# Performance work log

Measured on AMD Instinct MI355X. Metric: run time of the kernel, lower is better.

## Reference

```python
import jax, jax.numpy as jnp
import numpy as np

EPS = 1e-6
TEMPERATURE = 0.75
SINKHORN_ITERS = 7


def setup_inputs() -> dict:
    key = jax.random.key(0)
    ks = jax.random.split(key, 6)
    b, h, t, d_h = 4, 8, 4096, 64
    bs = 256
    nb = t // bs
    q = jax.random.normal(ks[0], (b, h, t, d_h), jnp.float32)
    k = jax.random.normal(ks[1], (b, h, t, d_h), jnp.float32)
    v = jax.random.normal(ks[2], (b, h, t, d_h), jnp.float32)
    # uniform noise for gumbel sampling in the sinkhorn sort net
    gumbel_u = jax.random.uniform(ks[3], (b * h, nb, nb), jnp.float32,
                                  minval=EPS, maxval=1.0 - EPS)
    W_out = jax.random.normal(ks[4], (2 * d_h, d_h), jnp.float32) / np.sqrt(2 * d_h)
    b_out = jnp.zeros((d_h,), jnp.float32)
    return {"q": q, "k": k, "v": v, "gumbel_u": gumbel_u,
            "W_out": W_out, "b_out": b_out, "bucket_size": bs}


def _sinkhorn(r, n_iters):
    # iterative row/col log-normalization of log-scores r: [bh, nb, nb]
    def body(r, _):
        r = r - jax.scipy.special.logsumexp(r, axis=2, keepdims=True)
        r = r - jax.scipy.special.logsumexp(r, axis=1, keepdims=True)
        return r, None
    r, _ = jax.lax.scan(body, r, None, length=n_iters)
    return jnp.exp(r)


def reference(q, k, v, gumbel_u, W_out, b_out, bucket_size):
    b, h, t, d_h = q.shape
    bh = b * h
    nb = t // bucket_size
    scale = d_h ** -0.5
    # merge batch/head and bucket: [bh, nb, bs, d_h]
    bq = q.reshape(bh, nb, bucket_size, d_h)
    bk = k.reshape(bh, nb, bucket_size, d_h)
    bv = v.reshape(bh, nb, bucket_size, d_h)
    # AttentionSortNet: bucket sums -> scores -> gumbel sinkhorn soft permutation
    q_sum = bq.sum(axis=2)  # [bh, nb, d_h]
    k_sum = bk.sum(axis=2)
    R0 = jax.nn.relu(jnp.einsum('bie,bje->bij', q_sum, k_sum) * scale)
    gumbel = -jnp.log(-jnp.log(gumbel_u + EPS) + EPS)
    r = (jnp.log(R0 + EPS) + gumbel) / TEMPERATURE
    R = _sinkhorn(r, SINKHORN_ITERS)  # [bh, nb, nb]
    # soft-reorder k/v buckets with R
    k_r = jnp.einsum('bij,bjsd->bisd', R, bk)
    v_r = jnp.einsum('bij,bjsd->bisd', R, bv)
    # local (within-bucket) attention
    local_s = jnp.einsum('bnie,bnje->bnij', bq, bk) * scale
    local_out = jnp.einsum('bnij,bnjd->bnid', jax.nn.softmax(local_s, axis=-1), bv)
    # attention over soft-sorted buckets
    sort_s = jnp.einsum('bnie,bnje->bnij', bq, k_r) * scale
    sort_out = jnp.einsum('bnij,bnjd->bnid', jax.nn.softmax(sort_s, axis=-1), v_r)
    # concat local + sorted heads, project 2*d_h -> d_h
    out = jnp.concatenate([local_out, sort_out], axis=-1)  # [bh, nb, bs, 2*d_h]
    out = out @ W_out + b_out
    return out.reshape(b, h, t, d_h)
```

## Files before the change

kernel.cpp:

```cpp
#include <hip/hip_runtime.h>
#include <math.h>


typedef __attribute__((ext_vector_type(8))) short short8;
typedef __attribute__((ext_vector_type(4))) float f32x4;

constexpr int BH = 32;
constexpr int NB = 16;
constexpr int BS = 256;
constexpr int D  = 64;
constexpr int BUCKET = BS * D;
constexpr float SCALE = 0.125f;

__device__ inline unsigned bf16_rne_u(float x) {
  unsigned u = __builtin_bit_cast(unsigned, x);
  return (u + 0x7FFFu + ((u >> 16) & 1u)) >> 16;
}
__device__ inline unsigned cvt2_bf16(float a, float b) {
  return bf16_rne_u(a) | (bf16_rne_u(b) << 16);
}
__device__ inline void split_pair(float a, float b, unsigned& uhi, unsigned& ulo) {
  uhi = cvt2_bf16(a, b);
  float ha = __builtin_bit_cast(float, uhi << 16);
  float hb = __builtin_bit_cast(float, uhi & 0xFFFF0000u);
  ulo = cvt2_bf16(a - ha, b - hb);
}

__global__ __launch_bounds__(256) void k_bucket_sums(
    const float* __restrict__ q, const float* __restrict__ k,
    float* __restrict__ qsum, float* __restrict__ ksum) {
  const int bid = blockIdx.x;
  const int t = threadIdx.x;
  const int c4 = t & 15;
  const int rg = t >> 4;
  const float4* qb = (const float4*)(q + (size_t)bid * BUCKET);
  const float4* kb = (const float4*)(k + (size_t)bid * BUCKET);
  float4 sq = make_float4(0.f, 0.f, 0.f, 0.f);
  float4 sk = make_float4(0.f, 0.f, 0.f, 0.f);
  for (int s = rg; s < BS; s += 16) {
    float4 a = qb[s * 16 + c4];
    float4 b2 = kb[s * 16 + c4];
    sq.x += a.x; sq.y += a.y; sq.z += a.z; sq.w += a.w;
    sk.x += b2.x; sk.y += b2.y; sk.z += b2.z; sk.w += b2.w;
  }
  __shared__ float red[2][16][64];
  *(float4*)&red[0][rg][4 * c4] = sq;
  *(float4*)&red[1][rg][4 * c4] = sk;
  __syncthreads();
  if (t < 128) {
    const int which = t >> 6;
    const int d = t & 63;
    float s = 0.f;
    #pragma unroll
    for (int g2 = 0; g2 < 16; ++g2) s += red[which][g2][d];
    (which ? ksum : qsum)[bid * D + d] = s;
  }
}

__global__ __launch_bounds__(256) void k_sinkhorn(
    const float* __restrict__ qsum, const float* __restrict__ ksum,
    const float* __restrict__ gu, float* __restrict__ R) {
  const int bh = blockIdx.x;
  const int t = threadIdx.x;
  const int i = t >> 4, j = t & 15;
  __shared__ float qs[16][64], ks[16][64], r[16][17];
  for (int idx = t; idx < NB * D; idx += 256) {
    qs[idx >> 6][idx & 63] = qsum[bh * NB * D + idx];
    ks[idx >> 6][idx & 63] = ksum[bh * NB * D + idx];
  }
  __syncthreads();
  float dot = 0.f;
  #pragma unroll
  for (int e = 0; e < D; ++e) dot += qs[i][e] * ks[j][e];
  const float R0 = fmaxf(dot * SCALE, 0.f);
  const float u = gu[bh * 256 + t];
  const float g = -logf(-logf(u + 1e-6f) + 1e-6f);
  float rv = (logf(R0 + 1e-6f) + g) * (1.0f / 0.75f);
  r[i][j] = rv;
  __syncthreads();
  for (int it = 0; it < 7; ++it) {
    float m = -1e30f;
    #pragma unroll
    for (int jj = 0; jj < 16; ++jj) m = fmaxf(m, r[i][jj]);
    float ssum = 0.f;
    #pragma unroll
    for (int jj = 0; jj < 16; ++jj) ssum += expf(r[i][jj] - m);
    float nv = r[i][j] - (m + logf(ssum));
    __syncthreads();
    r[i][j] = nv;
    __syncthreads();
    m = -1e30f;
    #pragma unroll
    for (int ii = 0; ii < 16; ++ii) m = fmaxf(m, r[ii][j]);
    ssum = 0.f;
    #pragma unroll
    for (int ii = 0; ii < 16; ++ii) ssum += expf(r[ii][j] - m);
    nv = r[i][j] - (m + logf(ssum));
    __syncthreads();
    r[i][j] = nv;
    __syncthreads();
  }
  R[bh * 256 + t] = expf(r[i][j]);
}

__global__ __launch_bounds__(256, 4) void k_mix(
    const float* __restrict__ k, const float* __restrict__ v,
    const float* __restrict__ R,
    float* __restrict__ kr, float* __restrict__ vr) {
  const int bid = blockIdx.x;
  const int bh = bid >> 5;
  const int ch = bid & 31;
  const int t = threadIdx.x;
  __shared__ float Rs[16][16];
  Rs[t >> 4][t & 15] = R[bh * 256 + t];
  __syncthreads();
  const int f = ch * 256 + t;
  const float2* kb = (const float2*)(k + (size_t)bh * NB * BUCKET);
  const float2* vb = (const float2*)(v + (size_t)bh * NB * BUCKET);
  float2 ka[16], va[16];
  #pragma unroll
  for (int i = 0; i < 16; ++i) {
    ka[i] = make_float2(0.f, 0.f);
    va[i] = make_float2(0.f, 0.f);
  }
  #pragma unroll
  for (int j = 0; j < 16; ++j) {
    const float2 kv = kb[j * 8192 + f];
    const float2 vv = vb[j * 8192 + f];
    #pragma unroll
    for (int i = 0; i < 16; ++i) {
      const float w = Rs[i][j];
      ka[i].x += w * kv.x; ka[i].y += w * kv.y;
      va[i].x += w * vv.x; va[i].y += w * vv.y;
    }
  }
  float2* kro = (float2*)(kr + (size_t)bh * NB * BUCKET);
  float2* vro = (float2*)(vr + (size_t)bh * NB * BUCKET);
  #pragma unroll
  for (int i = 0; i < 16; ++i) {
    kro[i * 8192 + f] = ka[i];
    vro[i * 8192 + f] = va[i];
  }
}

__global__ __launch_bounds__(256, 2) void k_attn(
    const float* __restrict__ q,
    const float* __restrict__ k,  const float* __restrict__ v,
    const float* __restrict__ kr, const float* __restrict__ vr,
    const float* __restrict__ Wp, const float* __restrict__ bp,
    float* __restrict__ out) {
  const int bid = blockIdx.x;
  const int t = threadIdx.x;
  const int wv = t >> 6;
  const int lane = t & 63;
  const int g = lane >> 4;
  const int c = lane & 15;
  const size_t boff = (size_t)bid * BUCKET;

  __shared__ unsigned short Khi[32 * 72], Klo[32 * 72];
  __shared__ unsigned short VThi[64 * 40], VTlo[64 * 40];
  __shared__ unsigned short Pbh[4][16 * 40], Pbl[4][16 * 40];

  short8 Qhi[4][2], Qlo[4][2];
  #pragma unroll
  for (int qm = 0; qm < 4; ++qm) {
    #pragma unroll
    for (int ks = 0; ks < 2; ++ks) {
      const float* src = q + boff + (size_t)(64 * wv + 16 * qm + c) * D + 32 * ks + 8 * g;
      float4 a = *(const float4*)src;
      float4 b2 = *(const float4*)(src + 4);
      unsigned h0, l0, h1, l1, h2, l2, h3, l3;
      split_pair(a.x * SCALE, a.y * SCALE, h0, l0);
      split_pair(a.z * SCALE, a.w * SCALE, h1, l1);
      split_pair(b2.x * SCALE, b2.y * SCALE, h2, l2);
      split_pair(b2.z * SCALE, b2.w * SCALE, h3, l3);
      uint4 uh = make_uint4(h0, h1, h2, h3);
      uint4 ul = make_uint4(l0, l1, l2, l3);
      Qhi[qm][ks] = __builtin_bit_cast(short8, uh);
      Qlo[qm][ks] = __builtin_bit_cast(short8, ul);
    }
  }

  unsigned short* ph = Pbh[wv];
  unsigned short* pl = Pbl[wv];

  f32x4 Pacc[4][4];
  #pragma unroll
  for (int qm = 0; qm < 4; ++qm)
    #pragma unroll
    for (int dn = 0; dn < 4; ++dn) Pacc[qm][dn] = (f32x4){0.f, 0.f, 0.f, 0.f};

  #pragma unroll
  for (int pass = 0; pass < 2; ++pass) {
    const float* kb = (pass ? kr : k) + boff;
    const float* vb = (pass ? vr : v) + boff;
    f32x4 Oacc[4][4];
    float lrow[4];
    #pragma unroll
    for (int qm = 0; qm < 4; ++qm) {
      lrow[qm] = 0.f;
      #pragma unroll
      for (int dn = 0; dn < 4; ++dn) Oacc[qm][dn] = (f32x4){0.f, 0.f, 0.f, 0.f};
    }

    for (int p = 0; p < 8; ++p) {
      __syncthreads();
      if (t < 128) {
        #pragma unroll
        for (int i = 0; i < 4; ++i) {
          int cell = t + 128 * i;
          int kkr = cell >> 4, dq = cell & 15;
          float4 a = *(const float4*)(kb + (size_t)(32 * p + kkr) * D + 4 * dq);
          unsigned h0, l0, h1, l1;
          split_pair(a.x, a.y, h0, l0);
          split_pair(a.z, a.w, h1, l1);
          *(uint2*)&Khi[kkr * 72 + 4 * dq] = make_uint2(h0, h1);
          *(uint2*)&Klo[kkr * 72 + 4 * dq] = make_uint2(l0, l1);
        }
      } else {
        int h2i = t - 128;
        int kkq = h2i >> 4, dq = h2i & 15;
        float4 rows[4];
        #pragma unroll
        for (int j = 0; j < 4; ++j)
          rows[j] = *(const float4*)(vb + (size_t)(32 * p + 4 * kkq + j) * D + 4 * dq);
        #pragma unroll
        for (int m = 0; m < 4; ++m) {
          float e0 = (m == 0) ? rows[0].x : (m == 1) ? rows[0].y : (m == 2) ? rows[0].z : rows[0].w;
          float e1 = (m == 0) ? rows[1].x : (m == 1) ? rows[1].y : (m == 2) ? rows[1].z : rows[1].w;
          float e2 = (m == 0) ? rows[2].x : (m == 1) ? rows[2].y : (m == 2) ? rows[2].z : rows[2].w;
          float e3 = (m == 0) ? rows[3].x : (m == 1) ? rows[3].y : (m == 2) ? rows[3].z : rows[3].w;
          unsigned h0, l0, h1, l1;
          split_pair(e0, e1, h0, l0);
          split_pair(e2, e3, h1, l1);
          *(uint2*)&VThi[(4 * dq + m) * 40 + 4 * kkq] = make_uint2(h0, h1);
          *(uint2*)&VTlo[(4 * dq + m) * 40 + 4 * kkq] = make_uint2(l0, l1);
        }
      }
      __syncthreads();

      f32x4 pe[4][2];
      #pragma unroll
      for (int kn = 0; kn < 2; ++kn) {
        f32x4 ST[4];
        #pragma unroll
        for (int qm = 0; qm < 4; ++qm) ST[qm] = (f32x4){0.f, 0.f, 0.f, 0.f};
        #pragma unroll
        for (int ks = 0; ks < 2; ++ks) {
          short8 KAhi = *(const short8*)&Khi[(16 * kn + c) * 72 + 32 * ks + 8 * g];
          short8 KAlo = *(const short8*)&Klo[(16 * kn + c) * 72 + 32 * ks + 8 * g];
          #pragma unroll
          for (int qm = 0; qm < 4; ++qm) {
            ST[qm] = __builtin_amdgcn_mfma_f32_16x16x32_bf16(KAhi, Qhi[qm][ks], ST[qm], 0, 0, 0);
            ST[qm] = __builtin_amdgcn_mfma_f32_16x16x32_bf16(KAhi, Qlo[qm][ks], ST[qm], 0, 0, 0);
            ST[qm] = __builtin_amdgcn_mfma_f32_16x16x32_bf16(KAlo, Qhi[qm][ks], ST[qm], 0, 0, 0);
          }
        }
        #pragma unroll
        for (int qm = 0; qm < 4; ++qm)
          #pragma unroll
          for (int r = 0; r < 4; ++r) pe[qm][kn][r] = __expf(ST[qm][r]);
      }

      #pragma unroll
      for (int qm = 0; qm < 4; ++qm) {
        lrow[qm] += ((pe[qm][0][0] + pe[qm][0][1]) + (pe[qm][0][2] + pe[qm][0][3]))
                  + ((pe[qm][1][0] + pe[qm][1][1]) + (pe[qm][1][2] + pe[qm][1][3]));
      }

      short8 Phi[4], Plo[4];
      #pragma unroll
      for (int qm = 0; qm < 4; ++qm) {
        #pragma unroll
        for (int kn = 0; kn < 2; ++kn) {
          unsigned h0, l0, h1, l1;
          split_pair(pe[qm][kn][0], pe[qm][kn][1], h0, l0);
          split_pair(pe[qm][kn][2], pe[qm][kn][3], h1, l1);
          *(uint2*)&ph[c * 40 + 16 * kn + 4 * g] = make_uint2(h0, h1);
          *(uint2*)&pl[c * 40 + 16 * kn + 4 * g] = make_uint2(l0, l1);
        }
        Phi[qm] = *(const short8*)&ph[c * 40 + 8 * g];
        Plo[qm] = *(const short8*)&pl[c * 40 + 8 * g];
      }

      #pragma unroll
      for (int dn = 0; dn < 4; ++dn) {
        short8 Vhi = *(const short8*)&VThi[(16 * dn + c) * 40 + 8 * g];
        short8 Vlo = *(const short8*)&VTlo[(16 * dn + c) * 40 + 8 * g];
        #pragma unroll
        for (int qm = 0; qm < 4; ++qm) {
          Oacc[qm][dn] = __builtin_amdgcn_mfma_f32_16x16x32_bf16(Phi[qm], Vhi, Oacc[qm][dn], 0, 0, 0);
          Oacc[qm][dn] = __builtin_amdgcn_mfma_f32_16x16x32_bf16(Phi[qm], Vlo, Oacc[qm][dn], 0, 0, 0);
          Oacc[qm][dn] = __builtin_amdgcn_mfma_f32_16x16x32_bf16(Plo[qm], Vhi, Oacc[qm][dn], 0, 0, 0);
        }
      }
    }

    f32x4 invs[4];
    #pragma unroll
    for (int qm = 0; qm < 4; ++qm) {
      float s = lrow[qm];
      s += __shfl_xor(s, 16, 64);
      s += __shfl_xor(s, 32, 64);
      #pragma unroll
      for (int r = 0; r < 4; ++r) invs[qm][r] = 1.0f / __shfl(s, 4 * g + r, 64);
    }

    #pragma unroll
    for (int ks2 = 0; ks2 < 2; ++ks2) {
      short8 Ahi[4], Alo[4];
      #pragma unroll
      for (int qm = 0; qm < 4; ++qm) {
        #pragma unroll
        for (int dnl = 0; dnl < 2; ++dnl) {
          const int dn = 2 * ks2 + dnl;
          unsigned uh0, ul0, uh1, ul1;
          split_pair(Oacc[qm][dn][0] * invs[qm][0], Oacc[qm][dn][1] * invs[qm][1], uh0, ul0);
          split_pair(Oacc[qm][dn][2] * invs[qm][2], Oacc[qm][dn][3] * invs[qm][3], uh1, ul1);
          const int base = 16 * dnl + c;
          ph[(4 * g + 0) * 40 + base] = (unsigned short)(uh0 & 0xFFFFu);
          ph[(4 * g + 1) * 40 + base] = (unsigned short)(uh0 >> 16);
          ph[(4 * g + 2) * 40 + base] = (unsigned short)(uh1 & 0xFFFFu);
          ph[(4 * g + 3) * 40 + base] = (unsigned short)(uh1 >> 16);
          pl[(4 * g + 0) * 40 + base] = (unsigned short)(ul0 & 0xFFFFu);
          pl[(4 * g + 1) * 40 + base] = (unsigned short)(ul0 >> 16);
          pl[(4 * g + 2) * 40 + base] = (unsigned short)(ul1 & 0xFFFFu);
          pl[(4 * g + 3) * 40 + base] = (unsigned short)(ul1 >> 16);
        }
        Ahi[qm] = *(const short8*)&ph[c * 40 + 8 * g];
        Alo[qm] = *(const short8*)&pl[c * 40 + 8 * g];
      }
      #pragma unroll
      for (int dn_o = 0; dn_o < 4; ++dn_o) {
        float wf[8];
        #pragma unroll
        for (int e = 0; e < 8; ++e)
          wf[e] = Wp[(size_t)(pass * 64 + 32 * ks2 + 8 * g + e) * 64 + 16 * dn_o + c];
        unsigned h0, l0, h1, l1, h2, l2, h3, l3;
        split_pair(wf[0], wf[1], h0, l0);
        split_pair(wf[2], wf[3], h1, l1);
        split_pair(wf[4], wf[5], h2, l2);
        split_pair(wf[6], wf[7], h3, l3);
        uint4 uh = make_uint4(h0, h1, h2, h3);
        uint4 ul = make_uint4(l0, l1, l2, l3);
        short8 WBhi = __builtin_bit_cast(short8, uh);
        short8 WBlo = __builtin_bit_cast(short8, ul);
        #pragma unroll
        for (int qm = 0; qm < 4; ++qm) {
          Pacc[qm][dn_o] = __builtin_amdgcn_mfma_f32_16x16x32_bf16(Ahi[qm], WBhi, Pacc[qm][dn_o], 0, 0, 0);
          Pacc[qm][dn_o] = __builtin_amdgcn_mfma_f32_16x16x32_bf16(Ahi[qm], WBlo, Pacc[qm][dn_o], 0, 0, 0);
          Pacc[qm][dn_o] = __builtin_amdgcn_mfma_f32_16x16x32_bf16(Alo[qm], WBhi, Pacc[qm][dn_o], 0, 0, 0);
        }
      }
    }
  }

  float bvals[4];
  #pragma unroll
  for (int dn_o = 0; dn_o < 4; ++dn_o) bvals[dn_o] = bp[16 * dn_o + c];
  #pragma unroll
  for (int qm = 0; qm < 4; ++qm)
    #pragma unroll
    for (int dn_o = 0; dn_o < 4; ++dn_o)
      #pragma unroll
      for (int r = 0; r < 4; ++r) {
        const int row = 64 * wv + 16 * qm + 4 * g + r;
        out[((size_t)bid * 256 + row) * 64 + 16 * dn_o + c] = Pacc[qm][dn_o][r] + bvals[dn_o];
      }
}

extern "C" void kernel_launch(void* const* d_in, const int* in_sizes, int n_in,
                              void* d_out, int out_size, void* d_ws, size_t ws_size,
                              hipStream_t stream) {
  (void)in_sizes; (void)n_in; (void)out_size; (void)ws_size;
  const float* q  = (const float*)d_in[0];
  const float* k  = (const float*)d_in[1];
  const float* v  = (const float*)d_in[2];
  const float* gu = (const float*)d_in[3];
  const float* W  = (const float*)d_in[4];
  const float* b  = (const float*)d_in[5];
  float* out = (float*)d_out;

  float* ws   = (float*)d_ws;
  float* R    = ws;
  float* qsum = ws + 8192;
  float* ksum = qsum + 32768;
  float* kr   = ksum + 32768;
  float* vr   = kr + 8388608;

  hipLaunchKernelGGL(k_bucket_sums, dim3(BH * NB), dim3(256), 0, stream, q, k, qsum, ksum);
  hipLaunchKernelGGL(k_sinkhorn,    dim3(BH),      dim3(256), 0, stream, qsum, ksum, gu, R);
  hipLaunchKernelGGL(k_mix,         dim3(BH * 32), dim3(256), 0, stream, k, v, R, kr, vr);
  hipLaunchKernelGGL(k_attn,        dim3(BH * NB), dim3(256), 0, stream,
                     q, k, v, kr, vr, W, b, out);
}
```

Before: 267.5 us.

## Precompute bf16 hi/lo split images of K/V and mixed K/V in producers

The bf16 hi/lo splitting of K and V moves out of the attention kernel's inner loads and into the producer kernels. The bucket-sum kernel now also writes split images of k and v, and the mix kernel writes its soft-sorted k/v directly as hi/lo bf16 pairs instead of fp32. The attention kernel then loads ready-made bf16 data, which avoids repeated conversion work, and the mixed k/v round trip keeps the same byte count. The costs are extra global writes for the unmixed k/v images and a larger workspace; if the workspace is too small, the unmixed pass falls back to fp32 loads.

Measured after the change: 295.7 us. 1.11x slower.

```diff
diff --git a/kernel.cpp b/kernel.cpp
--- a/kernel.cpp
+++ b/kernel.cpp
@@ -1,4 +1,5 @@
 #include <hip/hip_runtime.h>
+#include <hip/hip_bf16.h>
 #include <math.h>
 
 
@@ -12,36 +13,61 @@
 constexpr int BUCKET = BS * D;
 constexpr float SCALE = 0.125f;
 
-__device__ inline unsigned bf16_rne_u(float x) {
-  unsigned u = __builtin_bit_cast(unsigned, x);
-  return (u + 0x7FFFu + ((u >> 16) & 1u)) >> 16;
-}
-__device__ inline unsigned cvt2_bf16(float a, float b) {
-  return bf16_rne_u(a) | (bf16_rne_u(b) << 16);
+__device__ inline unsigned short f2bf(float x) {
+  __hip_bfloat16 h = __float2bfloat16(x);
+  unsigned short us;
+  __builtin_memcpy(&us, &h, 2);
+  return us;
+}
+__device__ inline unsigned pack_bf2(float a, float b) {
+  return (unsigned)f2bf(a) | ((unsigned)f2bf(b) << 16);
 }
 __device__ inline void split_pair(float a, float b, unsigned& uhi, unsigned& ulo) {
-  uhi = cvt2_bf16(a, b);
+  uhi = pack_bf2(a, b);
   float ha = __builtin_bit_cast(float, uhi << 16);
   float hb = __builtin_bit_cast(float, uhi & 0xFFFF0000u);
-  ulo = cvt2_bf16(a - ha, b - hb);
-}
-
-__global__ __launch_bounds__(256) void k_bucket_sums(
+  ulo = pack_bf2(a - ha, b - hb);
+}
+__device__ inline unsigned sel16(uint2 r, int m) {
+  unsigned w = (m < 2) ? r.x : r.y;
+  return (m & 1) ? (w >> 16) : (w & 0xFFFFu);
+}
+
+__global__ __launch_bounds__(256) void k_prep(
     const float* __restrict__ q, const float* __restrict__ k,
-    float* __restrict__ qsum, float* __restrict__ ksum) {
+    const float* __restrict__ v,
+    float* __restrict__ qsum, float* __restrict__ ksum,
+    unsigned* __restrict__ khi, unsigned* __restrict__ klo,
+    unsigned* __restrict__ vhi, unsigned* __restrict__ vlo,
+    int write_imgs) {
   const int bid = blockIdx.x;
   const int t = threadIdx.x;
   const int c4 = t & 15;
   const int rg = t >> 4;
   const float4* qb = (const float4*)(q + (size_t)bid * BUCKET);
   const float4* kb = (const float4*)(k + (size_t)bid * BUCKET);
+  const float4* vb = (const float4*)(v + (size_t)bid * BUCKET);
   float4 sq = make_float4(0.f, 0.f, 0.f, 0.f);
   float4 sk = make_float4(0.f, 0.f, 0.f, 0.f);
   for (int s = rg; s < BS; s += 16) {
-    float4 a = qb[s * 16 + c4];
-    float4 b2 = kb[s * 16 + c4];
+    const int f4 = s * 16 + c4;
+    float4 a = qb[f4];
+    float4 b2 = kb[f4];
     sq.x += a.x; sq.y += a.y; sq.z += a.z; sq.w += a.w;
     sk.x += b2.x; sk.y += b2.y; sk.z += b2.z; sk.w += b2.w;
+    if (write_imgs) {
+      const size_t u = 2 * ((size_t)bid * 4096 + f4);
+      unsigned h0, l0, h1, l1;
+      split_pair(b2.x, b2.y, h0, l0);
+      split_pair(b2.z, b2.w, h1, l1);
+      *(uint2*)&khi[u] = make_uint2(h0, h1);
+      *(uint2*)&klo[u] = make_uint2(l0, l1);
+      float4 c = vb[f4];
+      split_pair(c.x, c.y, h0, l0);
+      split_pair(c.z, c.w, h1, l1);
+      *(uint2*)&vhi[u] = make_uint2(h0, h1);
+      *(uint2*)&vlo[u] = make_uint2(l0, l1);
+    }
   }
   __shared__ float red[2][16][64];
   *(float4*)&red[0][rg][4 * c4] = sq;
@@ -106,7 +132,8 @@
 __global__ __launch_bounds__(256, 4) void k_mix(
     const float* __restrict__ k, const float* __restrict__ v,
     const float* __restrict__ R,
-    float* __restrict__ kr, float* __restrict__ vr) {
+    unsigned* __restrict__ krhi, unsigned* __restrict__ krlo,
+    unsigned* __restrict__ vrhi, unsigned* __restrict__ vrlo) {
   const int bid = blockIdx.x;
   const int bh = bid >> 5;
   const int ch = bid & 31;
@@ -134,19 +161,27 @@
       va[i].x += w * vv.x; va[i].y += w * vv.y;
     }
   }
-  float2* kro = (float2*)(kr + (size_t)bh * NB * BUCKET);
-  float2* vro = (float2*)(vr + (size_t)bh * NB * BUCKET);
+  const size_t ub = (size_t)bh * 131072 + f;
   #pragma unroll
   for (int i = 0; i < 16; ++i) {
-    kro[i * 8192 + f] = ka[i];
-    vro[i * 8192 + f] = va[i];
-  }
-}
-
+    unsigned h, l;
+    split_pair(ka[i].x, ka[i].y, h, l);
+    krhi[ub + i * 8192] = h;
+    krlo[ub + i * 8192] = l;
+    split_pair(va[i].x, va[i].y, h, l);
+    vrhi[ub + i * 8192] = h;
+    vrlo[ub + i * 8192] = l;
+  }
+}
+
+template <bool KV_IMG>
 __global__ __launch_bounds__(256, 2) void k_attn(
     const float* __restrict__ q,
     const float* __restrict__ k,  const float* __restrict__ v,
-    const float* __restrict__ kr, const float* __restrict__ vr,
+    const unsigned* __restrict__ khi, const unsigned* __restrict__ klo,
+    const unsigned* __restrict__ vhi, const unsigned* __restrict__ vlo,
+    const unsigned* __restrict__ krhi, const unsigned* __restrict__ krlo,
+    const unsigned* __restrict__ vrhi, const unsigned* __restrict__ vrlo,
     const float* __restrict__ Wp, const float* __restrict__ bp,
     float* __restrict__ out) {
   const int bid = blockIdx.x;
@@ -156,6 +191,7 @@
   const int g = lane >> 4;
   const int c = lane & 15;
   const size_t boff = (size_t)bid * BUCKET;
+  const size_t ub = (size_t)bid * 8192;
 
   __shared__ unsigned short Khi[32 * 72], Klo[32 * 72];
   __shared__ unsigned short VThi[64 * 40], VTlo[64 * 40];
@@ -192,8 +228,13 @@
 
   #pragma unroll
   for (int pass = 0; pass < 2; ++pass) {
-    const float* kb = (pass ? kr : k) + boff;
-    const float* vb = (pass ? vr : v) + boff;
+    const unsigned* bKhi = pass ? krhi : khi;
+    const unsigned* bKlo = pass ? krlo : klo;
+    const unsigned* bVhi = pass ? vrhi : vhi;
+    const unsigned* bVlo = pass ? vrlo : vlo;
+    const float* kb = (pass ? (const float*)nullptr : k + boff);
+    const float* vb = (pass ? (const float*)nullptr : v + boff);
+
     f32x4 Oacc[4][4];
     float lrow[4];
     #pragma unroll
@@ -205,36 +246,70 @@
 
     for (int p = 0; p < 8; ++p) {
       __syncthreads();
-      if (t < 128) {
-        #pragma unroll
-        for (int i = 0; i < 4; ++i) {
-          int cell = t + 128 * i;
-          int kkr = cell >> 4, dq = cell & 15;
-          float4 a = *(const float4*)(kb + (size_t)(32 * p + kkr) * D + 4 * dq);
-          unsigned h0, l0, h1, l1;
-          split_pair(a.x, a.y, h0, l0);
-          split_pair(a.z, a.w, h1, l1);
-          *(uint2*)&Khi[kkr * 72 + 4 * dq] = make_uint2(h0, h1);
-          *(uint2*)&Klo[kkr * 72 + 4 * dq] = make_uint2(l0, l1);
+      if (KV_IMG || pass == 1) {
+        if (t < 128) {
+          #pragma unroll
+          for (int i = 0; i < 4; ++i) {
+            int cell = t + 128 * i;
+            int kkr = cell >> 4, dq = cell & 15;
+            const size_t u = ub + (size_t)(32 * p + kkr) * 32 + 2 * dq;
+            *(uint2*)&Khi[kkr * 72 + 4 * dq] = *(const uint2*)&bKhi[u];
+            *(uint2*)&Klo[kkr * 72 + 4 * dq] = *(const uint2*)&bKlo[u];
+          }
+        } else {
+          int h2i = t - 128;
+          int kkq = h2i >> 4, dq = h2i & 15;
+          uint2 hr[4], lr[4];
+          #pragma unroll
+          for (int j = 0; j < 4; ++j) {
+            const size_t u = ub + (size_t)(32 * p + 4 * kkq + j) * 32 + 2 * dq;
+            hr[j] = *(const uint2*)&bVhi[u];
+            lr[j] = *(const uint2*)&bVlo[u];
+          }
+          #pragma unroll
+          for (int m = 0; m < 4; ++m) {
+            unsigned a0 = sel16(hr[0], m), a1 = sel16(hr[1], m);
+            unsigned a2 = sel16(hr[2], m), a3 = sel16(hr[3], m);
+            *(uint2*)&VThi[(4 * dq + m) * 40 + 4 * kkq] =
+                make_uint2(a0 | (a1 << 16), a2 | (a3 << 16));
+            a0 = sel16(lr[0], m); a1 = sel16(lr[1], m);
+            a2 = sel16(lr[2], m); a3 = sel16(lr[3], m);
+            *(uint2*)&VTlo[(4 * dq + m) * 40 + 4 * kkq] =
+                make_uint2(a0 | (a1 << 16), a2 | (a3 << 16));
+          }
         }
       } else {
-        int h2i = t - 128;
-        int kkq = h2i >> 4, dq = h2i & 15;
-        float4 rows[4];
-        #pragma unroll
-        for (int j = 0; j < 4; ++j)
-          rows[j] = *(const float4*)(vb + (size_t)(32 * p + 4 * kkq + j) * D + 4 * dq);
-        #pragma unroll
-        for (int m = 0; m < 4; ++m) {
-          float e0 = (m == 0) ? rows[0].x : (m == 1) ? rows[0].y : (m == 2) ? rows[0].z : rows[0].w;
-          float e1 = (m == 0) ? rows[1].x : (m == 1) ? rows[1].y : (m == 2) ? rows[1].z : rows[1].w;
-          float e2 = (m == 0) ? rows[2].x : (m == 1) ? rows[2].y : (m == 2) ? rows[2].z : rows[2].w;
-          float e3 = (m == 0) ? rows[3].x : (m == 1) ? rows[3].y : (m == 2) ? rows[3].z : rows[3].w;
-          unsigned h0, l0, h1, l1;
-          split_pair(e0, e1, h0, l0);
-          split_pair(e2, e3, h1, l1);
-          *(uint2*)&VThi[(4 * dq + m) * 40 + 4 * kkq] = make_uint2(h0, h1);
-          *(uint2*)&VTlo[(4 * dq + m) * 40 + 4 * kkq] = make_uint2(l0, l1);
+        if (t < 128) {
+          #pragma unroll
+          for (int i = 0; i < 4; ++i) {
+            int cell = t + 128 * i;
+            int kkr = cell >> 4, dq = cell & 15;
+            float4 a = *(const float4*)(kb + (size_t)(32 * p + kkr) * D + 4 * dq);
+            unsigned h0, l0, h1, l1;
+            split_pair(a.x, a.y, h0, l0);
+            split_pair(a.z, a.w, h1, l1);
+            *(uint2*)&Khi[kkr * 72 + 4 * dq] = make_uint2(h0, h1);
+            *(uint2*)&Klo[kkr * 72 + 4 * dq] = make_uint2(l0, l1);
+          }
+        } else {
+          int h2i = t - 128;
+          int kkq = h2i >> 4, dq = h2i & 15;
+          float4 rows[4];
+          #pragma unroll
+          for (int j = 0; j < 4; ++j)
+            rows[j] = *(const float4*)(vb + (size_t)(32 * p + 4 * kkq + j) * D + 4 * dq);
+          #pragma unroll
+          for (int m = 0; m < 4; ++m) {
+            float e0 = (m == 0) ? rows[0].x : (m == 1) ? rows[0].y : (m == 2) ? rows[0].z : rows[0].w;
+            float e1 = (m == 0) ? rows[1].x : (m == 1) ? rows[1].y : (m == 2) ? rows[1].z : rows[1].w;
+            float e2 = (m == 0) ? rows[2].x : (m == 1) ? rows[2].y : (m == 2) ? rows[2].z : rows[2].w;
+            float e3 = (m == 0) ? rows[3].x : (m == 1) ? rows[3].y : (m == 2) ? rows[3].z : rows[3].w;
+            unsigned h0, l0, h1, l1;
+            split_pair(e0, e1, h0, l0);
+            split_pair(e2, e3, h1, l1);
+            *(uint2*)&VThi[(4 * dq + m) * 40 + 4 * kkq] = make_uint2(h0, h1);
+            *(uint2*)&VTlo[(4 * dq + m) * 40 + 4 * kkq] = make_uint2(l0, l1);
+          }
         }
       }
       __syncthreads();
@@ -285,13 +360,13 @@
 
       #pragma unroll
       for (int dn = 0; dn < 4; ++dn) {
-        short8 Vhi = *(const short8*)&VThi[(16 * dn + c) * 40 + 8 * g];
-        short8 Vlo = *(const short8*)&VTlo[(16 * dn + c) * 40 + 8 * g];
+        short8 Vhi2 = *(const short8*)&VThi[(16 * dn + c) * 40 + 8 * g];
+        short8 Vlo2 = *(const short8*)&VTlo[(16 * dn + c) * 40 + 8 * g];
         #pragma unroll
         for (int qm = 0; qm < 4; ++qm) {
-          Oacc[qm][dn] = __builtin_amdgcn_mfma_f32_16x16x32_bf16(Phi[qm], Vhi, Oacc[qm][dn], 0, 0, 0);
-          Oacc[qm][dn] = __builtin_amdgcn_mfma_f32_16x16x32_bf16(Phi[qm], Vlo, Oacc[qm][dn], 0, 0, 0);
-          Oacc[qm][dn] = __builtin_amdgcn_mfma_f32_16x16x32_bf16(Plo[qm], Vhi, Oacc[qm][dn], 0, 0, 0);
+          Oacc[qm][dn] = __builtin_amdgcn_mfma_f32_16x16x32_bf16(Phi[qm], Vhi2, Oacc[qm][dn], 0, 0, 0);
+          Oacc[qm][dn] = __builtin_amdgcn_mfma_f32_16x16x32_bf16(Phi[qm], Vlo2, Oacc[qm][dn], 0, 0, 0);
+          Oacc[qm][dn] = __builtin_amdgcn_mfma_f32_16x16x32_bf16(Plo[qm], Vhi2, Oacc[qm][dn], 0, 0, 0);
         }
       }
     }
@@ -372,7 +447,7 @@
 extern "C" void kernel_launch(void* const* d_in, const int* in_sizes, int n_in,
                               void* d_out, int out_size, void* d_ws, size_t ws_size,
                               hipStream_t stream) {
-  (void)in_sizes; (void)n_in; (void)out_size; (void)ws_size;
+  (void)in_sizes; (void)n_in; (void)out_size;
   const float* q  = (const float*)d_in[0];
   const float* k  = (const float*)d_in[1];
   const float* v  = (const float*)d_in[2];
@@ -381,16 +456,31 @@
   const float* b  = (const float*)d_in[5];
   float* out = (float*)d_out;
 
-  float* ws   = (float*)d_ws;
-  float* R    = ws;
-  float* qsum = ws + 8192;
-  float* ksum = qsum + 32768;
-  float* kr   = ksum + 32768;
-  float* vr   = kr + 8388608;
-
-  hipLaunchKernelGGL(k_bucket_sums, dim3(BH * NB), dim3(256), 0, stream, q, k, qsum, ksum);
-  hipLaunchKernelGGL(k_sinkhorn,    dim3(BH),      dim3(256), 0, stream, qsum, ksum, gu, R);
-  hipLaunchKernelGGL(k_mix,         dim3(BH * 32), dim3(256), 0, stream, k, v, R, kr, vr);
-  hipLaunchKernelGGL(k_attn,        dim3(BH * NB), dim3(256), 0, stream,
-                     q, k, v, kr, vr, W, b, out);
-}
+  float* ws    = (float*)d_ws;
+  float* R     = ws;
+  float* qsum  = ws + 8192;
+  float* ksum  = qsum + 32768;
+  unsigned* krhi = (unsigned*)(ksum + 32768);
+  unsigned* krlo = krhi + 4194304;
+  unsigned* vrhi = krlo + 4194304;
+  unsigned* vrlo = vrhi + 4194304;
+  unsigned* khi  = vrlo + 4194304;
+  unsigned* klo  = khi + 4194304;
+  unsigned* vhi  = klo + 4194304;
+  unsigned* vlo  = vhi + 4194304;
+  const size_t need_img = (size_t)73728 * 4 + (size_t)8 * 4194304 * 4;
+  const bool img = ws_size >= need_img;
+
+  hipLaunchKernelGGL(k_prep,     dim3(BH * NB), dim3(256), 0, stream,
+                     q, k, v, qsum, ksum, khi, klo, vhi, vlo, img ? 1 : 0);
+  hipLaunchKernelGGL(k_sinkhorn, dim3(BH),      dim3(256), 0, stream, qsum, ksum, gu, R);
+  hipLaunchKernelGGL(k_mix,      dim3(BH * 32), dim3(256), 0, stream,
+                     k, v, R, krhi, krlo, vrhi, vrlo);
+  if (img) {
+    hipLaunchKernelGGL((k_attn<true>),  dim3(BH * NB), dim3(256), 0, stream,
+                       q, k, v, khi, klo, vhi, vlo, krhi, krlo, vrhi, vrlo, W, b, out);
+  } else {
+    hipLaunchKernelGGL((k_attn<false>), dim3(BH * NB), dim3(256), 0, stream,
+                       q, k, v, khi, klo, vhi, vlo, krhi, krlo, vrhi, vrlo, W, b, out);
+  }
+}
```
